# Performance work log

Hardware: AMD Instinct MI355X
Metric: run time of the kernel (lower is better)

## Reference

```python
import jax, jax.numpy as jnp
import numpy as np

N = 1024      # num_nodes
D = 64        # input/hidden/output feature dim
IDX = 64      # idx_dim
H = 8         # msg MLP width
L = 3         # num_layers


def setup_inputs() -> dict:
    key = jax.random.key(0)
    ks = jax.random.split(key, 10)
    return {
        "y": jax.random.normal(ks[0], (N, D), jnp.float32),
        "adj": jax.random.uniform(ks[1], (N, N), jnp.float32),
        "adj_deriv": jax.random.normal(ks[2], (N, N), jnp.float32),
        "t_grad": jax.random.normal(ks[3], (N, N), jnp.float32),
        "idx_emb": jax.random.normal(ks[4], (N, IDX), jnp.float32),
        # stacked params for the two msg MLPs (index 0 = adj, 1 = adj_derivative)
        "msg_W1": jax.random.normal(ks[5], (2, H, 2 * IDX + 1), jnp.float32) / np.float32(np.sqrt(2 * IDX + 1)),
        "msg_b1": jnp.zeros((2, H), jnp.float32),
        "msg_W2": jax.random.normal(ks[6], (2, H, H), jnp.float32) / np.float32(np.sqrt(H)),
        "msg_b2": jnp.zeros((2, H), jnp.float32),
        "msg_W3": jax.random.normal(ks[7], (2, 1, H), jnp.float32) / np.float32(np.sqrt(H)),
        "msg_b3": jnp.zeros((2, 1), jnp.float32),
        # per-layer fusion weights: [A@x, A.T@x, dA@x, dA.T@x, x] -> 5 matrices
        "gnn_W": jax.random.normal(ks[8], (L, 5, D, D), jnp.float32) / np.float32(np.sqrt(D)),
        "gnn_b": jnp.zeros((L, D), jnp.float32),
    }


def _msg_mlp(a, idx_emb, W1, b1, W2, b2, W3, b3):
    # Edge-wise 2-hidden-layer relu MLP over concat([a_ij, emb_i, emb_j]).
    # Split W1 so the [N,N,2*IDX+1] concat is never materialized.
    w_a = W1[:, 0]                 # [H]
    w_i = W1[:, 1:1 + IDX]         # [H, IDX]
    w_j = W1[:, 1 + IDX:]          # [H, IDX]
    row = idx_emb @ w_i.T          # [N, H]
    col = idx_emb @ w_j.T          # [N, H]
    h = jax.nn.relu(a[:, :, None] * w_a + row[:, None, :] + col[None, :, :] + b1)  # [N,N,H]
    h = jax.nn.relu(jnp.einsum('nmh,kh->nmk', h, W2) + b2)                          # [N,N,H]
    out = jnp.einsum('nmh,oh->nmo', h, W3) + b3                                     # [N,N,1]
    return out[..., 0]


def reference(y, adj, adj_deriv, t_grad, idx_emb, msg_W1, msg_b1, msg_W2, msg_b2,
              msg_W3, msg_b3, gnn_W, gnn_b):
    # enc_idx=True: reweight adjacency and its derivative with the edge-wise MLPs
    a = _msg_mlp(adj, idx_emb, msg_W1[0], msg_b1[0], msg_W2[0], msg_b2[0], msg_W3[0], msg_b3[0])
    ad = _msg_mlp(adj_deriv, idx_emb, msg_W1[1], msg_b1[1], msg_W2[1], msg_b2[1], msg_W3[1], msg_b3[1])

    x = y
    for l in range(L):
        W, b = gnn_W[l], gnn_b[l]
        x = ((a @ x) @ W[0] + (a.T @ x) @ W[1]
             + (ad @ x) @ W[2] + (ad.T @ x) @ W[3]
             + x @ W[4] + b)
        if l < L - 1:
            x = jax.nn.relu(x)

    tg = jnp.mean(t_grad, axis=0)          # [N]
    return tg[:, None] * x                 # einsum('i,ij->ij')
```

## Files before the change

kernel.cpp:

```cpp
#include <hip/hip_runtime.h>

typedef __attribute__((ext_vector_type(8))) short bf16x8;
typedef __attribute__((ext_vector_type(4))) float f32x4;
typedef __attribute__((ext_vector_type(4))) unsigned short us4;

__device__ __forceinline__ unsigned short f2bf(float f) {
    unsigned int u = __builtin_bit_cast(unsigned int, f);
    unsigned int r = (u + 0x7fffu + ((u >> 16) & 1u)) >> 16;
    return (unsigned short)r;
}

__global__ __launch_bounds__(256) void k_aux(
    const float* __restrict__ idx_emb, const float* __restrict__ msg_W1,
    float* __restrict__ rc,
    const float* __restrict__ t_grad, float* __restrict__ tg,
    const float* __restrict__ y, unsigned short* __restrict__ xbf,
    const float* __restrict__ gnn_W, unsigned short* __restrict__ WbfT) {
    __shared__ float red[4][64];
    int bx = blockIdx.x, t = threadIdx.x;
    if (bx < 128) {
        int tid = bx * 256 + t;
        int h = tid & 7, n = (tid >> 3) & 1023, t_ = (tid >> 13) & 1, k = tid >> 14;
        const float* wv = msg_W1 + k * 1032 + h * 129 + 1 + t_ * 64;
        const float* e = idx_emb + n * 64;
        float s = 0.f;
#pragma unroll
        for (int d = 0; d < 64; ++d) s += e[d] * wv[d];
        rc[(k * 2 + t_) * 8192 + n * 8 + h] = s;
    } else if (bx < 144) {
        int jl = t & 63, sg = t >> 6;
        int j = (bx - 128) * 64 + jl;
        float acc = 0.f;
        for (int i = 0; i < 256; ++i) acc += t_grad[(sg * 256 + i) * 1024 + j];
        red[sg][jl] = acc;
        __syncthreads();
        if (sg == 0)
            tg[j] = (red[0][jl] + red[1][jl] + red[2][jl] + red[3][jl]) * (1.f / 1024.f);
    } else if (bx < 160) {
        int base = (bx - 144) * 4096 + t;
#pragma unroll
        for (int p = 0; p < 16; ++p) xbf[base + p * 256] = f2bf(y[base + p * 256]);
    } else if (bx < 175) {
        int wi = bx - 160;
        const float* src = gnn_W + wi * 4096;
        unsigned short* dst = WbfT + wi * 4096;
        int c = t & 63, dg = t >> 6;
#pragma unroll
        for (int p = 0; p < 16; ++p) {
            int d = dg + p * 4;
            dst[c * 64 + d] = f2bf(src[d * 64 + c]);
        }
    }
}

__global__ __launch_bounds__(256) void k_msgcvt(
    const float* __restrict__ adj, const float* __restrict__ adj_deriv,
    const float* __restrict__ W1, const float* __restrict__ b1,
    const float* __restrict__ W2, const float* __restrict__ b2,
    const float* __restrict__ W3, const float* __restrict__ b3,
    const float* __restrict__ rc, unsigned short* __restrict__ Abf) {
    int mt = blockIdx.x, nt = blockIdx.y, z = blockIdx.z;
    const float* A = z ? adj_deriv : adj;
    unsigned short* D0 = Abf + z * 2097152;
    unsigned short* D1 = D0 + 1048576;
    int k = z;

    float wa[8], b1v[8], w2[64], b2v[8], w3v[8];
#pragma unroll
    for (int h = 0; h < 8; ++h) {
        wa[h]  = W1[k * 1032 + h * 129];
        b1v[h] = b1[k * 8 + h];
        b2v[h] = b2[k * 8 + h];
        w3v[h] = W3[k * 8 + h];
    }
#pragma unroll
    for (int i = 0; i < 64; ++i) w2[i] = W2[k * 64 + i];
    float b3v = b3[k];

    int t = threadIdx.x;
    int c = t & 63, rg = t >> 6;
    const float* colp = rc + (k * 2 + 1) * 8192 + (mt * 64 + c) * 8;
    float cm[8];
    *(float4*)&cm[0] = *(const float4*)colp;
    *(float4*)&cm[4] = *(const float4*)(colp + 4);
    const float* rowp = rc + (k * 2) * 8192 + (nt * 64) * 8;

    __shared__ unsigned short tile[64][65];
#pragma unroll
    for (int p = 0; p < 16; ++p) {
        int r = rg + 4 * p;
        float av = A[(nt * 64 + r) * 1024 + mt * 64 + c];
        float rn[8];
        *(float4*)&rn[0] = *(const float4*)(rowp + r * 8);
        *(float4*)&rn[4] = *(const float4*)(rowp + r * 8 + 4);
        float h1[8];
#pragma unroll
        for (int h = 0; h < 8; ++h) {
            float v = av * wa[h] + rn[h] + cm[h] + b1v[h];
            h1[h] = v > 0.f ? v : 0.f;
        }
        float o = b3v;
#pragma unroll
        for (int kk = 0; kk < 8; ++kk) {
            float s = b2v[kk];
#pragma unroll
            for (int h = 0; h < 8; ++h) s += h1[h] * w2[kk * 8 + h];
            s = s > 0.f ? s : 0.f;
            o += s * w3v[kk];
        }
        unsigned short us = f2bf(o);
        D0[(nt * 64 + r) * 1024 + mt * 64 + c] = us;
        tile[r][c] = us;
    }
    __syncthreads();
#pragma unroll
    for (int p = 0; p < 16; ++p) {
        int r = rg + 4 * p;
        D1[(mt * 64 + r) * 1024 + nt * 64 + c] = tile[c][r];
    }
}

__global__ __launch_bounds__(256) void k_gemm2(
    const unsigned short* __restrict__ Abf,
    const unsigned short* __restrict__ xbf,
    const unsigned short* __restrict__ WT,
    float* __restrict__ u4, float* __restrict__ P) {
    int nt = blockIdx.x, ms = blockIdx.y;
    int t = threadIdx.x, w = t >> 6, l = t & 63;
    int lr = l & 15, lk = l >> 4, klo = 8 * lk;
    int m0 = ms * 64;
    __shared__ unsigned short uTs[16384];

    int mrow = m0 + w * 16 + lr;
    bf16x8 xa[2];
    xa[0] = *(const bf16x8*)&xbf[mrow * 64 + klo];
    xa[1] = *(const bf16x8*)&xbf[mrow * 64 + 32 + klo];
    int njmax = (nt == 0) ? 5 : 4;
    for (int j = 0; j < njmax; ++j) {
        f32x4 au[4];
#pragma unroll
        for (int cf = 0; cf < 4; ++cf) au[cf] = (f32x4){0.f, 0.f, 0.f, 0.f};
#pragma unroll
        for (int kk = 0; kk < 2; ++kk)
#pragma unroll
            for (int cf = 0; cf < 4; ++cf) {
                bf16x8 wf = *(const bf16x8*)&WT[(j * 64 + cf * 16 + lr) * 64 + kk * 32 + klo];
                au[cf] = __builtin_amdgcn_mfma_f32_16x16x32_bf16(xa[kk], wf, au[cf], 0, 0, 0);
            }
        if (j < 4) {
#pragma unroll
            for (int cf = 0; cf < 4; ++cf) {
                int cc = cf * 16 + lr;
                us4 pk;
                pk[0] = f2bf(au[cf][0]); pk[1] = f2bf(au[cf][1]);
                pk[2] = f2bf(au[cf][2]); pk[3] = f2bf(au[cf][3]);
                int off = ((j * 64 + cc) * 64 + w * 16 + lk * 4) * 2;
                *(us4*)((char*)uTs + (off ^ ((cc & 7) << 4))) = pk;
            }
        } else {
#pragma unroll
            for (int cf = 0; cf < 4; ++cf)
#pragma unroll
                for (int r = 0; r < 4; ++r)
                    u4[(m0 + w * 16 + lk * 4 + r) * 64 + cf * 16 + lr] = au[cf][r];
        }
    }
    __syncthreads();

    f32x4 acc[4];
#pragma unroll
    for (int cf = 0; cf < 4; ++cf) acc[cf] = (f32x4){0.f, 0.f, 0.f, 0.f};
    int arow = nt * 64 + w * 16 + lr;
#pragma unroll
    for (int j = 0; j < 4; ++j) {
#pragma unroll
        for (int kk = 0; kk < 2; ++kk) {
            bf16x8 af = *(const bf16x8*)&Abf[j * 1048576 + arow * 1024 + m0 + kk * 32 + klo];
#pragma unroll
            for (int cf = 0; cf < 4; ++cf) {
                int cc = cf * 16 + lr;
                int off = ((j * 64 + cc) * 64 + kk * 32 + klo) * 2;
                bf16x8 bfr = *(const bf16x8*)((char*)uTs + (off ^ ((cc & 7) << 4)));
                acc[cf] = __builtin_amdgcn_mfma_f32_16x16x32_bf16(af, bfr, acc[cf], 0, 0, 0);
            }
        }
    }
    float* Pp = P + ms * 65536;
    int nbase = nt * 64 + w * 16 + lk * 4;
#pragma unroll
    for (int cf = 0; cf < 4; ++cf)
#pragma unroll
        for (int r = 0; r < 4; ++r)
            Pp[(nbase + r) * 64 + cf * 16 + lr] = acc[cf][r];
}

__global__ void k_post(const float* __restrict__ P, const float* __restrict__ u4,
                       const float* __restrict__ b, const float* __restrict__ tg,
                       float* __restrict__ out, unsigned short* __restrict__ xbf,
                       int mode) {
    int idx = blockIdx.x * 256 + threadIdx.x;
    int n = idx >> 6, c = idx & 63;
    float s = u4[idx] + b[c];
#pragma unroll
    for (int k = 0; k < 16; ++k) s += P[k * 65536 + idx];
    if (mode < 2) {
        s = fmaxf(s, 0.f);
        xbf[idx] = f2bf(s);
    } else {
        out[idx] = tg[n] * s;
    }
}

extern "C" void kernel_launch(void* const* d_in, const int* in_sizes, int n_in,
                              void* d_out, int out_size, void* d_ws, size_t ws_size,
                              hipStream_t stream) {
    const float* y         = (const float*)d_in[0];
    const float* adj       = (const float*)d_in[1];
    const float* adj_deriv = (const float*)d_in[2];
    const float* t_grad    = (const float*)d_in[3];
    const float* idx_emb   = (const float*)d_in[4];
    const float* msg_W1    = (const float*)d_in[5];
    const float* msg_b1    = (const float*)d_in[6];
    const float* msg_W2    = (const float*)d_in[7];
    const float* msg_b2    = (const float*)d_in[8];
    const float* msg_W3    = (const float*)d_in[9];
    const float* msg_b3    = (const float*)d_in[10];
    const float* gnn_W     = (const float*)d_in[11];
    const float* gnn_b     = (const float*)d_in[12];

    float* ws = (float*)d_ws;
    float* rc  = ws;
    float* tg  = ws + 32768;
    float* u4  = ws + 33792;
    float* P   = ws + 99328;
    unsigned short* xbf  = (unsigned short*)(ws + 1147904);
    unsigned short* WbfT = (unsigned short*)(ws + 1180672);
    unsigned short* Abf  = (unsigned short*)(ws + 1211392);

    k_aux<<<175, 256, 0, stream>>>(idx_emb, msg_W1, rc, t_grad, tg,
                                   y, xbf, gnn_W, WbfT);
    k_msgcvt<<<dim3(16, 16, 2), 256, 0, stream>>>(adj, adj_deriv,
                                                  msg_W1, msg_b1, msg_W2, msg_b2,
                                                  msg_W3, msg_b3, rc, Abf);
    for (int l = 0; l < 3; ++l) {
        k_gemm2<<<dim3(16, 16), 256, 0, stream>>>(Abf, xbf, WbfT + l * 20480, u4, P);
        k_post<<<256, 256, 0, stream>>>(P, u4, gnn_b + l * 64, tg,
                                        (float*)d_out, xbf, (l < 2) ? l : 2);
    }
}
```

Measured before the change: 66.04 us.

## Fuse per-layer post-reduction and ReLU into next layer's GEMM kernel prologue

Removes the separate k_post launches between layers. Each layer kernel now reduces the previous layer's 16 split-K partials, adds the bias, applies ReLU and converts to bf16 straight into shared memory. P and u4 are double-buffered so a layer does not overwrite partials it is still reading. This saves two launches and the xbf round trip, but every one of the 256 blocks re-reads 16 partial slices for its 64-row strip. That is 16x redundant reading of the partial buffers across the nt dimension.

```diff
diff --git a/kernel.cpp b/kernel.cpp
--- a/kernel.cpp
+++ b/kernel.cpp
@@ -120,33 +120,66 @@
     }
 }
 
-__global__ __launch_bounds__(256) void k_gemm2(
+template<int L>
+__global__ __launch_bounds__(256) void k_layer(
     const unsigned short* __restrict__ Abf,
     const unsigned short* __restrict__ xbf,
+    const float* __restrict__ Pin, const float* __restrict__ u4in,
+    const float* __restrict__ bprev,
     const unsigned short* __restrict__ WT,
-    float* __restrict__ u4, float* __restrict__ P) {
+    float* __restrict__ u4out, float* __restrict__ Pout) {
     int nt = blockIdx.x, ms = blockIdx.y;
-    int t = threadIdx.x, w = t >> 6, l = t & 63;
-    int lr = l & 15, lk = l >> 4, klo = 8 * lk;
+    int t = threadIdx.x, w = t >> 6, l64 = t & 63;
+    int lr = l64 & 15, lk = l64 >> 4, klo = 8 * lk;
     int m0 = ms * 64;
     __shared__ unsigned short uTs[16384];
-
-    int mrow = m0 + w * 16 + lr;
-    bf16x8 xa[2];
-    xa[0] = *(const bf16x8*)&xbf[mrow * 64 + klo];
-    xa[1] = *(const bf16x8*)&xbf[mrow * 64 + 32 + klo];
+    __shared__ unsigned short xs[4096];
+
+    if constexpr (L == 0) {
+#pragma unroll
+        for (int p = 0; p < 2; ++p) {
+            int e = (t + p * 256) * 8;
+            *(bf16x8*)&xs[e] = *(const bf16x8*)&xbf[m0 * 64 + e];
+        }
+    } else {
+#pragma unroll
+        for (int p = 0; p < 4; ++p) {
+            int q = t + p * 256;
+            int row = q >> 4, c4 = (q & 15) * 4;
+            int gi = (m0 + row) * 64 + c4;
+            float4 acc4 = *(const float4*)&u4in[gi];
+            float4 b4 = *(const float4*)&bprev[c4];
+            acc4.x += b4.x; acc4.y += b4.y; acc4.z += b4.z; acc4.w += b4.w;
+#pragma unroll
+            for (int s = 0; s < 16; ++s) {
+                float4 pv = *(const float4*)&Pin[s * 65536 + gi];
+                acc4.x += pv.x; acc4.y += pv.y; acc4.z += pv.z; acc4.w += pv.w;
+            }
+            us4 pk;
+            pk[0] = f2bf(fmaxf(acc4.x, 0.f));
+            pk[1] = f2bf(fmaxf(acc4.y, 0.f));
+            pk[2] = f2bf(fmaxf(acc4.z, 0.f));
+            pk[3] = f2bf(fmaxf(acc4.w, 0.f));
+            *(us4*)&xs[row * 64 + c4] = pk;
+        }
+    }
+    __syncthreads();
+
+    int mloc = w * 16 + lr;
+    bf16x8 xa0 = *(const bf16x8*)&xs[mloc * 64 + klo];
+    bf16x8 xa1 = *(const bf16x8*)&xs[mloc * 64 + 32 + klo];
     int njmax = (nt == 0) ? 5 : 4;
     for (int j = 0; j < njmax; ++j) {
         f32x4 au[4];
 #pragma unroll
         for (int cf = 0; cf < 4; ++cf) au[cf] = (f32x4){0.f, 0.f, 0.f, 0.f};
 #pragma unroll
-        for (int kk = 0; kk < 2; ++kk)
-#pragma unroll
-            for (int cf = 0; cf < 4; ++cf) {
-                bf16x8 wf = *(const bf16x8*)&WT[(j * 64 + cf * 16 + lr) * 64 + kk * 32 + klo];
-                au[cf] = __builtin_amdgcn_mfma_f32_16x16x32_bf16(xa[kk], wf, au[cf], 0, 0, 0);
-            }
+        for (int cf = 0; cf < 4; ++cf) {
+            bf16x8 wf0 = *(const bf16x8*)&WT[(j * 64 + cf * 16 + lr) * 64 + klo];
+            bf16x8 wf1 = *(const bf16x8*)&WT[(j * 64 + cf * 16 + lr) * 64 + 32 + klo];
+            au[cf] = __builtin_amdgcn_mfma_f32_16x16x32_bf16(xa0, wf0, au[cf], 0, 0, 0);
+            au[cf] = __builtin_amdgcn_mfma_f32_16x16x32_bf16(xa1, wf1, au[cf], 0, 0, 0);
+        }
         if (j < 4) {
 #pragma unroll
             for (int cf = 0; cf < 4; ++cf) {
@@ -162,7 +195,7 @@
             for (int cf = 0; cf < 4; ++cf)
 #pragma unroll
                 for (int r = 0; r < 4; ++r)
-                    u4[(m0 + w * 16 + lk * 4 + r) * 64 + cf * 16 + lr] = au[cf][r];
+                    u4out[(m0 + w * 16 + lk * 4 + r) * 64 + cf * 16 + lr] = au[cf][r];
         }
     }
     __syncthreads();
@@ -185,7 +218,7 @@
             }
         }
     }
-    float* Pp = P + ms * 65536;
+    float* Pp = Pout + ms * 65536;
     int nbase = nt * 64 + w * 16 + lk * 4;
 #pragma unroll
     for (int cf = 0; cf < 4; ++cf)
@@ -194,21 +227,15 @@
             Pp[(nbase + r) * 64 + cf * 16 + lr] = acc[cf][r];
 }
 
-__global__ void k_post(const float* __restrict__ P, const float* __restrict__ u4,
-                       const float* __restrict__ b, const float* __restrict__ tg,
-                       float* __restrict__ out, unsigned short* __restrict__ xbf,
-                       int mode) {
+__global__ void k_final(const float* __restrict__ P, const float* __restrict__ u4,
+                        const float* __restrict__ b, const float* __restrict__ tg,
+                        float* __restrict__ out) {
     int idx = blockIdx.x * 256 + threadIdx.x;
     int n = idx >> 6, c = idx & 63;
     float s = u4[idx] + b[c];
 #pragma unroll
     for (int k = 0; k < 16; ++k) s += P[k * 65536 + idx];
-    if (mode < 2) {
-        s = fmaxf(s, 0.f);
-        xbf[idx] = f2bf(s);
-    } else {
-        out[idx] = tg[n] * s;
-    }
+    out[idx] = tg[n] * s;
 }
 
 extern "C" void kernel_launch(void* const* d_in, const int* in_sizes, int n_in,
@@ -227,24 +254,29 @@
     const float* msg_b3    = (const float*)d_in[10];
     const float* gnn_W     = (const float*)d_in[11];
     const float* gnn_b     = (const float*)d_in[12];
+    float* outp = (float*)d_out;
 
     float* ws = (float*)d_ws;
-    float* rc  = ws;
-    float* tg  = ws + 32768;
-    float* u4  = ws + 33792;
-    float* P   = ws + 99328;
-    unsigned short* xbf  = (unsigned short*)(ws + 1147904);
-    unsigned short* WbfT = (unsigned short*)(ws + 1180672);
-    unsigned short* Abf  = (unsigned short*)(ws + 1211392);
+    float* rc   = ws;
+    float* tg   = ws + 32768;
+    float* u4A  = ws + 33792;
+    float* u4B  = ws + 99328;
+    float* PA   = ws + 164864;
+    float* PB   = ws + 1213440;
+    unsigned short* xbf  = (unsigned short*)(ws + 2262016);
+    unsigned short* WbfT = (unsigned short*)(ws + 2294784);
+    unsigned short* Abf  = (unsigned short*)(ws + 2325504);
 
     k_aux<<<175, 256, 0, stream>>>(idx_emb, msg_W1, rc, t_grad, tg,
                                    y, xbf, gnn_W, WbfT);
     k_msgcvt<<<dim3(16, 16, 2), 256, 0, stream>>>(adj, adj_deriv,
                                                   msg_W1, msg_b1, msg_W2, msg_b2,
                                                   msg_W3, msg_b3, rc, Abf);
-    for (int l = 0; l < 3; ++l) {
-        k_gemm2<<<dim3(16, 16), 256, 0, stream>>>(Abf, xbf, WbfT + l * 20480, u4, P);
-        k_post<<<256, 256, 0, stream>>>(P, u4, gnn_b + l * 64, tg,
-                                        (float*)d_out, xbf, (l < 2) ? l : 2);
-    }
-}
+    k_layer<0><<<dim3(16, 16), 256, 0, stream>>>(Abf, xbf, PA, u4A, gnn_b,
+                                                 WbfT, u4A, PA);
+    k_layer<1><<<dim3(16, 16), 256, 0, stream>>>(Abf, xbf, PA, u4A, gnn_b,
+                                                 WbfT + 20480, u4B, PB);
+    k_layer<2><<<dim3(16, 16), 256, 0, stream>>>(Abf, xbf, PB, u4B, gnn_b + 64,
+                                                 WbfT + 40960, u4A, PA);
+    k_final<<<256, 256, 0, stream>>>(PA, u4A, gnn_b + 128, tg, outp);
+}
```

Measured after the change: 73.10 us. +10.7%, slower.

## Fuse per-layer GEMM and post-reduction via software grid barrier

Applied to the files above, without the earlier changes.

Merges the per-layer GEMM kernel and the split-K reduction/activation kernel into one kernel that synchronizes all 256 blocks with an atomic-counter grid barrier. This removes three kernel launches and their inter-kernel gaps. Input and output activation buffers are ping-ponged, and a memset clears the barrier counters each call. It relies on all 256 blocks being co-resident, and it adds a spin-wait plus system-scope atomics and a memset launch.

```diff
diff --git a/kernel.cpp b/kernel.cpp
--- a/kernel.cpp
+++ b/kernel.cpp
@@ -8,6 +8,19 @@
     unsigned int u = __builtin_bit_cast(unsigned int, f);
     unsigned int r = (u + 0x7fffu + ((u >> 16) & 1u)) >> 16;
     return (unsigned short)r;
+}
+
+__device__ __forceinline__ void gbar(unsigned int* ctr) {
+    __syncthreads();
+    if (threadIdx.x == 0) {
+        __builtin_amdgcn_fence(__ATOMIC_SEQ_CST, "");
+        __hip_atomic_fetch_add(ctr, 1u, __ATOMIC_RELEASE, __HIP_MEMORY_SCOPE_SYSTEM);
+        while (__hip_atomic_load(ctr, __ATOMIC_ACQUIRE,
+                                 __HIP_MEMORY_SCOPE_SYSTEM) < 256u)
+            __builtin_amdgcn_s_sleep(2);
+    }
+    __syncthreads();
+    __builtin_amdgcn_fence(__ATOMIC_ACQUIRE, "");
 }
 
 __global__ __launch_bounds__(256) void k_aux(
@@ -120,33 +133,37 @@
     }
 }
 
-__global__ __launch_bounds__(256) void k_gemm2(
+template<int L>
+__global__ __launch_bounds__(256, 1) void k_layerfull(
     const unsigned short* __restrict__ Abf,
-    const unsigned short* __restrict__ xbf,
+    const unsigned short* __restrict__ xin,
     const unsigned short* __restrict__ WT,
-    float* __restrict__ u4, float* __restrict__ P) {
+    const float* __restrict__ bvec,
+    const float* __restrict__ tg,
+    float* __restrict__ u4, float* __restrict__ P,
+    unsigned short* __restrict__ xout, float* __restrict__ out,
+    unsigned int* __restrict__ bar) {
     int nt = blockIdx.x, ms = blockIdx.y;
-    int t = threadIdx.x, w = t >> 6, l = t & 63;
-    int lr = l & 15, lk = l >> 4, klo = 8 * lk;
+    int t = threadIdx.x, w = t >> 6, l64 = t & 63;
+    int lr = l64 & 15, lk = l64 >> 4, klo = 8 * lk;
     int m0 = ms * 64;
     __shared__ unsigned short uTs[16384];
 
     int mrow = m0 + w * 16 + lr;
-    bf16x8 xa[2];
-    xa[0] = *(const bf16x8*)&xbf[mrow * 64 + klo];
-    xa[1] = *(const bf16x8*)&xbf[mrow * 64 + 32 + klo];
+    bf16x8 xa0 = *(const bf16x8*)&xin[mrow * 64 + klo];
+    bf16x8 xa1 = *(const bf16x8*)&xin[mrow * 64 + 32 + klo];
     int njmax = (nt == 0) ? 5 : 4;
     for (int j = 0; j < njmax; ++j) {
         f32x4 au[4];
 #pragma unroll
         for (int cf = 0; cf < 4; ++cf) au[cf] = (f32x4){0.f, 0.f, 0.f, 0.f};
 #pragma unroll
-        for (int kk = 0; kk < 2; ++kk)
-#pragma unroll
-            for (int cf = 0; cf < 4; ++cf) {
-                bf16x8 wf = *(const bf16x8*)&WT[(j * 64 + cf * 16 + lr) * 64 + kk * 32 + klo];
-                au[cf] = __builtin_amdgcn_mfma_f32_16x16x32_bf16(xa[kk], wf, au[cf], 0, 0, 0);
-            }
+        for (int cf = 0; cf < 4; ++cf) {
+            bf16x8 wf0 = *(const bf16x8*)&WT[(j * 64 + cf * 16 + lr) * 64 + klo];
+            bf16x8 wf1 = *(const bf16x8*)&WT[(j * 64 + cf * 16 + lr) * 64 + 32 + klo];
+            au[cf] = __builtin_amdgcn_mfma_f32_16x16x32_bf16(xa0, wf0, au[cf], 0, 0, 0);
+            au[cf] = __builtin_amdgcn_mfma_f32_16x16x32_bf16(xa1, wf1, au[cf], 0, 0, 0);
+        }
         if (j < 4) {
 #pragma unroll
             for (int cf = 0; cf < 4; ++cf) {
@@ -192,22 +209,22 @@
 #pragma unroll
         for (int r = 0; r < 4; ++r)
             Pp[(nbase + r) * 64 + cf * 16 + lr] = acc[cf][r];
-}
-
-__global__ void k_post(const float* __restrict__ P, const float* __restrict__ u4,
-                       const float* __restrict__ b, const float* __restrict__ tg,
-                       float* __restrict__ out, unsigned short* __restrict__ xbf,
-                       int mode) {
-    int idx = blockIdx.x * 256 + threadIdx.x;
-    int n = idx >> 6, c = idx & 63;
-    float s = u4[idx] + b[c];
-#pragma unroll
-    for (int k = 0; k < 16; ++k) s += P[k * 65536 + idx];
-    if (mode < 2) {
-        s = fmaxf(s, 0.f);
-        xbf[idx] = f2bf(s);
-    } else {
-        out[idx] = tg[n] * s;
+
+    gbar(bar);
+
+    {
+        int bid = blockIdx.y * 16 + blockIdx.x;
+        int idx = bid * 256 + t;
+        int n = idx >> 6, c = idx & 63;
+        float s = u4[idx] + bvec[c];
+#pragma unroll
+        for (int k2 = 0; k2 < 16; ++k2) s += P[k2 * 65536 + idx];
+        if (L < 2) {
+            s = fmaxf(s, 0.f);
+            xout[idx] = f2bf(s);
+        } else {
+            out[idx] = tg[n] * s;
+        }
     }
 }
 
@@ -227,24 +244,32 @@
     const float* msg_b3    = (const float*)d_in[10];
     const float* gnn_W     = (const float*)d_in[11];
     const float* gnn_b     = (const float*)d_in[12];
+    float* outp = (float*)d_out;
 
     float* ws = (float*)d_ws;
-    float* rc  = ws;
-    float* tg  = ws + 32768;
-    float* u4  = ws + 33792;
-    float* P   = ws + 99328;
-    unsigned short* xbf  = (unsigned short*)(ws + 1147904);
-    unsigned short* WbfT = (unsigned short*)(ws + 1180672);
-    unsigned short* Abf  = (unsigned short*)(ws + 1211392);
-
+    unsigned int* bar = (unsigned int*)ws;
+    float* rc   = ws + 64;
+    float* tg   = ws + 32832;
+    float* u4   = ws + 33856;
+    float* P    = ws + 99392;
+    unsigned short* xbfA = (unsigned short*)(ws + 1147968);
+    unsigned short* xbfB = (unsigned short*)(ws + 1180736);
+    unsigned short* WbfT = (unsigned short*)(ws + 1213504);
+    unsigned short* Abf  = (unsigned short*)(ws + 1244224);
+
+    hipMemsetAsync(bar, 0, 64, stream);
     k_aux<<<175, 256, 0, stream>>>(idx_emb, msg_W1, rc, t_grad, tg,
-                                   y, xbf, gnn_W, WbfT);
+                                   y, xbfA, gnn_W, WbfT);
     k_msgcvt<<<dim3(16, 16, 2), 256, 0, stream>>>(adj, adj_deriv,
                                                   msg_W1, msg_b1, msg_W2, msg_b2,
                                                   msg_W3, msg_b3, rc, Abf);
-    for (int l = 0; l < 3; ++l) {
-        k_gemm2<<<dim3(16, 16), 256, 0, stream>>>(Abf, xbf, WbfT + l * 20480, u4, P);
-        k_post<<<256, 256, 0, stream>>>(P, u4, gnn_b + l * 64, tg,
-                                        (float*)d_out, xbf, (l < 2) ? l : 2);
-    }
-}
+    k_layerfull<0><<<dim3(16, 16), 256, 0, stream>>>(Abf, xbfA, WbfT,
+                                                     gnn_b, tg, u4, P,
+                                                     xbfB, outp, &bar[0]);
+    k_layerfull<1><<<dim3(16, 16), 256, 0, stream>>>(Abf, xbfB, WbfT + 20480,
+                                                     gnn_b + 64, tg, u4, P,
+                                                     xbfA, outp, &bar[1]);
+    k_layerfull<2><<<dim3(16, 16), 256, 0, stream>>>(Abf, xbfA, WbfT + 40960,
+                                                     gnn_b + 128, tg, u4, P,
+                                                     xbfB, outp, &bar[2]);
+}
```

Measured after the change: 159.7 us. +141.8%, slower.

## Restructure GNN layers into row-stripe kernels fusing reduction, epilogue and next-layer projection

Applied to the files above, without the earlier changes.

Replaces the per-layer gemm+split-K partial buffer+post kernel pair with one stripe kernel per layer. Each block owns 8 output rows, reduces the full K across its four waves in LDS, and applies bias, ReLU and the tg scale. It then computes the next layer's x@W projections (uT) for those rows in the epilogue. The first layer's uT projection is folded into the message-MLP kernel as extra blocks. This removes the 16-way partial-sum buffer traffic, the separate post kernel and the recomputation of uT in every gemm block. The cost is only 128 blocks, each using half of a 16-row MFMA tile, plus more global reads of uT per block.

```diff
diff --git a/kernel.cpp b/kernel.cpp
--- a/kernel.cpp
+++ b/kernel.cpp
@@ -53,161 +53,204 @@
     }
 }
 
-__global__ __launch_bounds__(256) void k_msgcvt(
+__global__ __launch_bounds__(256) void k_msgu(
     const float* __restrict__ adj, const float* __restrict__ adj_deriv,
     const float* __restrict__ W1, const float* __restrict__ b1,
     const float* __restrict__ W2, const float* __restrict__ b2,
     const float* __restrict__ W3, const float* __restrict__ b3,
-    const float* __restrict__ rc, unsigned short* __restrict__ Abf) {
-    int mt = blockIdx.x, nt = blockIdx.y, z = blockIdx.z;
-    const float* A = z ? adj_deriv : adj;
-    unsigned short* D0 = Abf + z * 2097152;
-    unsigned short* D1 = D0 + 1048576;
-    int k = z;
-
-    float wa[8], b1v[8], w2[64], b2v[8], w3v[8];
-#pragma unroll
-    for (int h = 0; h < 8; ++h) {
-        wa[h]  = W1[k * 1032 + h * 129];
-        b1v[h] = b1[k * 8 + h];
-        b2v[h] = b2[k * 8 + h];
-        w3v[h] = W3[k * 8 + h];
-    }
-#pragma unroll
-    for (int i = 0; i < 64; ++i) w2[i] = W2[k * 64 + i];
-    float b3v = b3[k];
-
-    int t = threadIdx.x;
-    int c = t & 63, rg = t >> 6;
-    const float* colp = rc + (k * 2 + 1) * 8192 + (mt * 64 + c) * 8;
-    float cm[8];
-    *(float4*)&cm[0] = *(const float4*)colp;
-    *(float4*)&cm[4] = *(const float4*)(colp + 4);
-    const float* rowp = rc + (k * 2) * 8192 + (nt * 64) * 8;
-
-    __shared__ unsigned short tile[64][65];
-#pragma unroll
-    for (int p = 0; p < 16; ++p) {
-        int r = rg + 4 * p;
-        float av = A[(nt * 64 + r) * 1024 + mt * 64 + c];
-        float rn[8];
-        *(float4*)&rn[0] = *(const float4*)(rowp + r * 8);
-        *(float4*)&rn[4] = *(const float4*)(rowp + r * 8 + 4);
-        float h1[8];
+    const float* __restrict__ rc, unsigned short* __restrict__ Abf,
+    const unsigned short* __restrict__ xbf,
+    const unsigned short* __restrict__ WbfT,
+    unsigned short* __restrict__ uT0) {
+    int bx = blockIdx.x, t = threadIdx.x;
+    if (bx < 512) {
+        int mt = bx & 15, nt = (bx >> 4) & 15, z = bx >> 8;
+        const float* A = z ? adj_deriv : adj;
+        unsigned short* D0 = Abf + z * 2097152;
+        unsigned short* D1 = D0 + 1048576;
+        int k = z;
+
+        float wa[8], b1v[8], w2[64], b2v[8], w3v[8];
 #pragma unroll
         for (int h = 0; h < 8; ++h) {
-            float v = av * wa[h] + rn[h] + cm[h] + b1v[h];
-            h1[h] = v > 0.f ? v : 0.f;
-        }
-        float o = b3v;
-#pragma unroll
-        for (int kk = 0; kk < 8; ++kk) {
-            float s = b2v[kk];
-#pragma unroll
-            for (int h = 0; h < 8; ++h) s += h1[h] * w2[kk * 8 + h];
-            s = s > 0.f ? s : 0.f;
-            o += s * w3v[kk];
-        }
-        unsigned short us = f2bf(o);
-        D0[(nt * 64 + r) * 1024 + mt * 64 + c] = us;
-        tile[r][c] = us;
-    }
-    __syncthreads();
-#pragma unroll
-    for (int p = 0; p < 16; ++p) {
-        int r = rg + 4 * p;
-        D1[(mt * 64 + r) * 1024 + nt * 64 + c] = tile[c][r];
-    }
-}
-
-__global__ __launch_bounds__(256) void k_gemm2(
-    const unsigned short* __restrict__ Abf,
-    const unsigned short* __restrict__ xbf,
-    const unsigned short* __restrict__ WT,
-    float* __restrict__ u4, float* __restrict__ P) {
-    int nt = blockIdx.x, ms = blockIdx.y;
-    int t = threadIdx.x, w = t >> 6, l = t & 63;
-    int lr = l & 15, lk = l >> 4, klo = 8 * lk;
-    int m0 = ms * 64;
-    __shared__ unsigned short uTs[16384];
-
-    int mrow = m0 + w * 16 + lr;
-    bf16x8 xa[2];
-    xa[0] = *(const bf16x8*)&xbf[mrow * 64 + klo];
-    xa[1] = *(const bf16x8*)&xbf[mrow * 64 + 32 + klo];
-    int njmax = (nt == 0) ? 5 : 4;
-    for (int j = 0; j < njmax; ++j) {
-        f32x4 au[4];
-#pragma unroll
-        for (int cf = 0; cf < 4; ++cf) au[cf] = (f32x4){0.f, 0.f, 0.f, 0.f};
-#pragma unroll
-        for (int kk = 0; kk < 2; ++kk)
-#pragma unroll
-            for (int cf = 0; cf < 4; ++cf) {
-                bf16x8 wf = *(const bf16x8*)&WT[(j * 64 + cf * 16 + lr) * 64 + kk * 32 + klo];
-                au[cf] = __builtin_amdgcn_mfma_f32_16x16x32_bf16(xa[kk], wf, au[cf], 0, 0, 0);
-            }
-        if (j < 4) {
+            wa[h]  = W1[k * 1032 + h * 129];
+            b1v[h] = b1[k * 8 + h];
+            b2v[h] = b2[k * 8 + h];
+            w3v[h] = W3[k * 8 + h];
+        }
+#pragma unroll
+        for (int i = 0; i < 64; ++i) w2[i] = W2[k * 64 + i];
+        float b3v = b3[k];
+
+        int c = t & 63, rg = t >> 6;
+        const float* colp = rc + (k * 2 + 1) * 8192 + (mt * 64 + c) * 8;
+        float cm[8];
+        *(float4*)&cm[0] = *(const float4*)colp;
+        *(float4*)&cm[4] = *(const float4*)(colp + 4);
+        const float* rowp = rc + (k * 2) * 8192 + (nt * 64) * 8;
+
+        __shared__ unsigned short tile[64][65];
+#pragma unroll
+        for (int p = 0; p < 16; ++p) {
+            int r = rg + 4 * p;
+            float av = A[(nt * 64 + r) * 1024 + mt * 64 + c];
+            float rn[8];
+            *(float4*)&rn[0] = *(const float4*)(rowp + r * 8);
+            *(float4*)&rn[4] = *(const float4*)(rowp + r * 8 + 4);
+            float h1[8];
+#pragma unroll
+            for (int h = 0; h < 8; ++h) {
+                float v = av * wa[h] + rn[h] + cm[h] + b1v[h];
+                h1[h] = v > 0.f ? v : 0.f;
+            }
+            float o = b3v;
+#pragma unroll
+            for (int kk = 0; kk < 8; ++kk) {
+                float s = b2v[kk];
+#pragma unroll
+                for (int h = 0; h < 8; ++h) s += h1[h] * w2[kk * 8 + h];
+                s = s > 0.f ? s : 0.f;
+                o += s * w3v[kk];
+            }
+            unsigned short us = f2bf(o);
+            D0[(nt * 64 + r) * 1024 + mt * 64 + c] = us;
+            tile[r][c] = us;
+        }
+        __syncthreads();
+#pragma unroll
+        for (int p = 0; p < 16; ++p) {
+            int r = rg + 4 * p;
+            D1[(mt * 64 + r) * 1024 + nt * 64 + c] = tile[c][r];
+        }
+    } else {
+        int sb = bx - 512;
+        int w = t >> 6, l = t & 63, lr = l & 15, lk = l >> 4, klo = 8 * lk;
+        int m0 = sb * 64;
+        int mrow = m0 + w * 16 + lr;
+        bf16x8 xa0 = *(const bf16x8*)&xbf[mrow * 64 + klo];
+        bf16x8 xa1 = *(const bf16x8*)&xbf[mrow * 64 + 32 + klo];
+#pragma unroll
+        for (int j = 0; j < 4; ++j) {
+            f32x4 au[4];
+#pragma unroll
+            for (int cf = 0; cf < 4; ++cf) au[cf] = (f32x4){0.f, 0.f, 0.f, 0.f};
+#pragma unroll
+            for (int cf = 0; cf < 4; ++cf) {
+                bf16x8 wf0 = *(const bf16x8*)&WbfT[(j * 64 + cf * 16 + lr) * 64 + klo];
+                bf16x8 wf1 = *(const bf16x8*)&WbfT[(j * 64 + cf * 16 + lr) * 64 + 32 + klo];
+                au[cf] = __builtin_amdgcn_mfma_f32_16x16x32_bf16(xa0, wf0, au[cf], 0, 0, 0);
+                au[cf] = __builtin_amdgcn_mfma_f32_16x16x32_bf16(xa1, wf1, au[cf], 0, 0, 0);
+            }
 #pragma unroll
             for (int cf = 0; cf < 4; ++cf) {
                 int cc = cf * 16 + lr;
                 us4 pk;
                 pk[0] = f2bf(au[cf][0]); pk[1] = f2bf(au[cf][1]);
                 pk[2] = f2bf(au[cf][2]); pk[3] = f2bf(au[cf][3]);
-                int off = ((j * 64 + cc) * 64 + w * 16 + lk * 4) * 2;
-                *(us4*)((char*)uTs + (off ^ ((cc & 7) << 4))) = pk;
-            }
+                *(us4*)&uT0[(j * 64 + cc) * 1024 + m0 + w * 16 + lk * 4] = pk;
+            }
+        }
+    }
+}
+
+template<int L>
+__global__ __launch_bounds__(256) void k_stripe(
+    const unsigned short* __restrict__ Abf,
+    const unsigned short* __restrict__ uTin,
+    const unsigned short* __restrict__ xin,
+    const unsigned short* __restrict__ WbfT,
+    const float* __restrict__ gnn_b, const float* __restrict__ tg,
+    unsigned short* __restrict__ xout, unsigned short* __restrict__ uTout,
+    float* __restrict__ out) {
+    __shared__ float pLDS[4][16][64];
+    __shared__ unsigned short xns[8 * 72];
+    int t = threadIdx.x, w = t >> 6, l = t & 63;
+    int lr = l & 15, lk = l >> 4, klo = 8 * lk;
+    int r0 = blockIdx.x * 8;
+
+    f32x4 acc[4];
+#pragma unroll
+    for (int cf = 0; cf < 4; ++cf) acc[cf] = (f32x4){0.f, 0.f, 0.f, 0.f};
+
+    int arow = min(r0 + lr, 1023);
+#pragma unroll
+    for (int j = 0; j < 4; ++j) {
+        const unsigned short* Aj = Abf + j * 1048576 + arow * 1024;
+        const unsigned short* Uj = uTin + j * 65536;
+#pragma unroll
+        for (int ks = 0; ks < 8; ++ks) {
+            int kb = w * 256 + ks * 32;
+            bf16x8 af = *(const bf16x8*)&Aj[kb + klo];
+#pragma unroll
+            for (int cf = 0; cf < 4; ++cf) {
+                bf16x8 bfr = *(const bf16x8*)&Uj[(cf * 16 + lr) * 1024 + kb + klo];
+                acc[cf] = __builtin_amdgcn_mfma_f32_16x16x32_bf16(af, bfr, acc[cf], 0, 0, 0);
+            }
+        }
+    }
+    if (w == 0) {
+        const unsigned short* W4 = WbfT + L * 20480 + 16384;
+        const unsigned short* xr = xin + arow * 64;
+#pragma unroll
+        for (int kk = 0; kk < 2; ++kk) {
+            bf16x8 af = *(const bf16x8*)&xr[kk * 32 + klo];
+#pragma unroll
+            for (int cf = 0; cf < 4; ++cf) {
+                bf16x8 bfr = *(const bf16x8*)&W4[(cf * 16 + lr) * 64 + kk * 32 + klo];
+                acc[cf] = __builtin_amdgcn_mfma_f32_16x16x32_bf16(af, bfr, acc[cf], 0, 0, 0);
+            }
+        }
+    }
+#pragma unroll
+    for (int cf = 0; cf < 4; ++cf)
+#pragma unroll
+        for (int r = 0; r < 4; ++r)
+            pLDS[w][lk * 4 + r][cf * 16 + lr] = acc[cf][r];
+    __syncthreads();
+
+    const float* bv = gnn_b + L * 64;
+#pragma unroll
+    for (int p = 0; p < 2; ++p) {
+        int idx = t + p * 256;
+        int row = idx >> 6, col = idx & 63;
+        float s = pLDS[0][row][col] + pLDS[1][row][col] +
+                  pLDS[2][row][col] + pLDS[3][row][col] + bv[col];
+        if constexpr (L < 2) {
+            float v = fmaxf(s, 0.f);
+            unsigned short h = f2bf(v);
+            xout[(r0 + row) * 64 + col] = h;
+            xns[row * 72 + col] = h;
         } else {
-#pragma unroll
-            for (int cf = 0; cf < 4; ++cf)
-#pragma unroll
-                for (int r = 0; r < 4; ++r)
-                    u4[(m0 + w * 16 + lk * 4 + r) * 64 + cf * 16 + lr] = au[cf][r];
-        }
-    }
-    __syncthreads();
-
-    f32x4 acc[4];
-#pragma unroll
-    for (int cf = 0; cf < 4; ++cf) acc[cf] = (f32x4){0.f, 0.f, 0.f, 0.f};
-    int arow = nt * 64 + w * 16 + lr;
-#pragma unroll
-    for (int j = 0; j < 4; ++j) {
+            out[(r0 + row) * 64 + col] = tg[r0 + row] * s;
+        }
+    }
+
+    if constexpr (L < 2) {
+        __syncthreads();
+        const unsigned short* WTn = WbfT + (L + 1) * 20480;
+        int j = w;
+        f32x4 au[4];
+#pragma unroll
+        for (int cf = 0; cf < 4; ++cf) au[cf] = (f32x4){0.f, 0.f, 0.f, 0.f};
 #pragma unroll
         for (int kk = 0; kk < 2; ++kk) {
-            bf16x8 af = *(const bf16x8*)&Abf[j * 1048576 + arow * 1024 + m0 + kk * 32 + klo];
+            bf16x8 af = *(const bf16x8*)&xns[(lr & 7) * 72 + kk * 32 + klo];
+#pragma unroll
+            for (int cf = 0; cf < 4; ++cf) {
+                bf16x8 bfr = *(const bf16x8*)&WTn[(j * 64 + cf * 16 + lr) * 64 + kk * 32 + klo];
+                au[cf] = __builtin_amdgcn_mfma_f32_16x16x32_bf16(af, bfr, au[cf], 0, 0, 0);
+            }
+        }
+        if (lk < 2) {
 #pragma unroll
             for (int cf = 0; cf < 4; ++cf) {
                 int cc = cf * 16 + lr;
-                int off = ((j * 64 + cc) * 64 + kk * 32 + klo) * 2;
-                bf16x8 bfr = *(const bf16x8*)((char*)uTs + (off ^ ((cc & 7) << 4)));
-                acc[cf] = __builtin_amdgcn_mfma_f32_16x16x32_bf16(af, bfr, acc[cf], 0, 0, 0);
-            }
-        }
-    }
-    float* Pp = P + ms * 65536;
-    int nbase = nt * 64 + w * 16 + lk * 4;
-#pragma unroll
-    for (int cf = 0; cf < 4; ++cf)
-#pragma unroll
-        for (int r = 0; r < 4; ++r)
-            Pp[(nbase + r) * 64 + cf * 16 + lr] = acc[cf][r];
-}
-
-__global__ void k_post(const float* __restrict__ P, const float* __restrict__ u4,
-                       const float* __restrict__ b, const float* __restrict__ tg,
-                       float* __restrict__ out, unsigned short* __restrict__ xbf,
-                       int mode) {
-    int idx = blockIdx.x * 256 + threadIdx.x;
-    int n = idx >> 6, c = idx & 63;
-    float s = u4[idx] + b[c];
-#pragma unroll
-    for (int k = 0; k < 16; ++k) s += P[k * 65536 + idx];
-    if (mode < 2) {
-        s = fmaxf(s, 0.f);
-        xbf[idx] = f2bf(s);
-    } else {
-        out[idx] = tg[n] * s;
+                us4 pk;
+                pk[0] = f2bf(au[cf][0]); pk[1] = f2bf(au[cf][1]);
+                pk[2] = f2bf(au[cf][2]); pk[3] = f2bf(au[cf][3]);
+                *(us4*)&uTout[(j * 64 + cc) * 1024 + r0 + lk * 4] = pk;
+            }
+        }
     }
 }
 
@@ -227,24 +270,28 @@
     const float* msg_b3    = (const float*)d_in[10];
     const float* gnn_W     = (const float*)d_in[11];
     const float* gnn_b     = (const float*)d_in[12];
+    float* outp = (float*)d_out;
 
     float* ws = (float*)d_ws;
-    float* rc  = ws;
-    float* tg  = ws + 32768;
-    float* u4  = ws + 33792;
-    float* P   = ws + 99328;
-    unsigned short* xbf  = (unsigned short*)(ws + 1147904);
-    unsigned short* WbfT = (unsigned short*)(ws + 1180672);
-    unsigned short* Abf  = (unsigned short*)(ws + 1211392);
+    float* rc = ws;
+    float* tg = ws + 32768;
+    unsigned short* xbfA = (unsigned short*)(ws + 33792);
+    unsigned short* xbfB = (unsigned short*)(ws + 66560);
+    unsigned short* WbfT = (unsigned short*)(ws + 99328);
+    unsigned short* uTA  = (unsigned short*)(ws + 130048);
+    unsigned short* uTB  = (unsigned short*)(ws + 261120);
+    unsigned short* Abf  = (unsigned short*)(ws + 392192);
 
     k_aux<<<175, 256, 0, stream>>>(idx_emb, msg_W1, rc, t_grad, tg,
-                                   y, xbf, gnn_W, WbfT);
-    k_msgcvt<<<dim3(16, 16, 2), 256, 0, stream>>>(adj, adj_deriv,
-                                                  msg_W1, msg_b1, msg_W2, msg_b2,
-                                                  msg_W3, msg_b3, rc, Abf);
-    for (int l = 0; l < 3; ++l) {
-        k_gemm2<<<dim3(16, 16), 256, 0, stream>>>(Abf, xbf, WbfT + l * 20480, u4, P);
-        k_post<<<256, 256, 0, stream>>>(P, u4, gnn_b + l * 64, tg,
-                                        (float*)d_out, xbf, (l < 2) ? l : 2);
-    }
-}
+                                   y, xbfA, gnn_W, WbfT);
+    k_msgu<<<528, 256, 0, stream>>>(adj, adj_deriv,
+                                    msg_W1, msg_b1, msg_W2, msg_b2,
+                                    msg_W3, msg_b3, rc, Abf,
+                                    xbfA, WbfT, uTA);
+    k_stripe<0><<<128, 256, 0, stream>>>(Abf, uTA, xbfA, WbfT, gnn_b, tg,
+                                         xbfB, uTB, outp);
+    k_stripe<1><<<128, 256, 0, stream>>>(Abf, uTB, xbfB, WbfT, gnn_b, tg,
+                                         xbfA, uTA, outp);
+    k_stripe<2><<<128, 256, 0, stream>>>(Abf, uTA, xbfA, WbfT, gnn_b, tg,
+                                         xbfB, uTB, outp);
+}
```

Result: slower. 113.8 us (+72.3%).
